# Optimization experiments

Measured on AMD Instinct MI355X. Metric: run time of the kernel, lower is better.

## Reference

```python
import jax, jax.numpy as jnp
import numpy as np
from math import exp, log

# Instant-NGP style multi-hash-grid constants (match init_kwargs)
BASE_RES = 16
MAX_RES = 2048
N_GRIDS = 16
LOG2_T = 19
TABLE_SIZE = 1 << LOG2_T  # power of two -> mod == low-bit mask
FEAT = 2
N_POINTS = 1_000_000

_pls = exp((log(MAX_RES) - log(BASE_RES)) / (N_GRIDS - 1))
RESOLUTIONS = np.floor(np.array([BASE_RES * _pls ** i for i in range(N_GRIDS)])).astype(np.float32)
# 8 voxel corner offsets, i-major (i*4 + j*2 + k) like the torch VOXEL_VTX_OFFSET
OFFSETS = np.array([[i, j, k] for i in (0, 1) for j in (0, 1) for k in (0, 1)], dtype=np.int32)
PRIMES = np.array([1, 2654435761, 805459861], dtype=np.uint32)


def setup_inputs() -> dict:
    key = jax.random.key(0)
    k1, k2 = jax.random.split(key)
    x = jax.random.normal(k1, (N_POINTS, 3), dtype=jnp.float32)
    # nn.init.uniform_(weight, a=-1e-4, b=1e-4)
    tables = jax.random.uniform(k2, (N_GRIDS, TABLE_SIZE, FEAT),
                                minval=-1e-4, maxval=1e-4, dtype=jnp.float32)
    return {"x": x, "tables": tables}


def _forward(x, tables):
    inbox = jnp.all((x >= -1.0) & (x <= 1.0), axis=-1)  # [B]
    offs = jnp.asarray(OFFSETS)                          # [8,3]
    primes = jnp.asarray(PRIMES)                         # [3] uint32
    res = jnp.asarray(RESOLUTIONS)                       # [G]
    # torch computes x_normed / interp weights under no_grad -> no grad to x
    xs = jax.lax.stop_gradient(x)

    def level(table, r):
        # (x - bbox_min) / (bbox_max - bbox_min) * resolution, bbox = [-1,1]^3
        xn = (xs + 1.0) * 0.5 * r                        # [B,3]
        v0 = jnp.floor(xn).astype(jnp.int32)             # [B,3]
        w = xn - v0.astype(jnp.float32)                  # [B,3] trilerp weights
        vidx = (v0[:, None, :] + offs[None]).astype(jnp.uint32)  # [B,8,3]
        # prime-XOR spatial hash; uint32 wraparound matches torch int64 math
        # modulo the power-of-two table size (low bits identical)
        h = (vidx[..., 0] * primes[0]) ^ (vidx[..., 1] * primes[1]) ^ (vidx[..., 2] * primes[2])
        h = (h & jnp.uint32(TABLE_SIZE - 1)).astype(jnp.int32)   # [B,8]
        feats = table[h]                                  # [B,8,F] gather
        # corner (i,j,k) weight = prod over dims of (w if bit else 1-w)
        wgt = jnp.prod(jnp.where(offs[None] == 1, w[:, None, :], 1.0 - w[:, None, :]), axis=-1)  # [B,8]
        c = jnp.einsum('bc,bcf->bf', wgt, feats)          # [B,F]
        return jnp.where(inbox[:, None], c, 0.0)          # out-of-bbox -> zeros

    per_level = jax.vmap(level)(tables, res)              # [G,B,F]
    B = x.shape[0]
    return jnp.transpose(per_level, (1, 0, 2)).reshape(B, N_GRIDS * FEAT)


def reference(x, tables):
    return _forward(x, tables)
```

## Files before the change

kernel.cpp:

```cpp
#include <hip/hip_runtime.h>
#include <hip/hip_bf16.h>
#include <math.h>

#define N_POINTS 1000000
#define N_GRIDS  16
#define LOG2_T   19
#define TABLE_MASK ((1u << LOG2_T) - 1u)
#define NBLOCKS  ((N_POINTS + 255) / 256)
#define CONV_BLOCKS 4096
#define FUSED_BLOCKS 2048
#define TAILB_BLOCKS 4096
#define N_ENTRIES (N_GRIDS << LOG2_T)
#define NCELL_AX 32
#define N_CELLS  (NCELL_AX * NCELL_AX * NCELL_AX)

struct ResArr { float r[N_GRIDS]; };

__device__ __forceinline__ unsigned pack_bf16x2(float a, float b)
{
    __hip_bfloat16 ha = __float2bfloat16(a);
    __hip_bfloat16 hb = __float2bfloat16(b);
    unsigned short ua = *(unsigned short*)&ha;
    unsigned short ub = *(unsigned short*)&hb;
    return (unsigned)ua | ((unsigned)ub << 16);
}

__device__ __forceinline__ float2 unpack_bf16x2(unsigned v)
{
    unsigned lo = (v & 0xffffu) << 16;
    unsigned hi = v & 0xffff0000u;
    return make_float2(__uint_as_float(lo), __uint_as_float(hi));
}

__device__ __forceinline__ unsigned expand_bits(unsigned v)
{
    v &= 0x3ffu;
    v = (v | (v << 16)) & 0x30000FFu;
    v = (v | (v << 8))  & 0x300F00Fu;
    v = (v | (v << 4))  & 0x30C30C3u;
    v = (v | (v << 2))  & 0x9249249u;
    return v;
}

__device__ __forceinline__ int morton_cell(float x0, float x1, float x2)
{
    int cx = (int)floorf((x0 + 1.f) * 16.f);
    int cy = (int)floorf((x1 + 1.f) * 16.f);
    int cz = (int)floorf((x2 + 1.f) * 16.f);
    cx = min(NCELL_AX - 1, max(0, cx));
    cy = min(NCELL_AX - 1, max(0, cy));
    cz = min(NCELL_AX - 1, max(0, cz));
    return (int)((expand_bits((unsigned)cx) << 2) |
                 (expand_bits((unsigned)cy) << 1) |
                  expand_bits((unsigned)cz));
}

__device__ __forceinline__ unsigned sel4(uint4 P, unsigned idx)
{
    const unsigned lo = (idx & 1u) ? P.y : P.x;
    const unsigned hi = (idx & 1u) ? P.w : P.z;
    return (idx & 2u) ? hi : lo;
}

__device__ __forceinline__ void gather_level_bf16(
    float x0, float x1, float x2, float r,
    const unsigned* __restrict__ tbl, float& c0, float& c1)
{
    const float xn0 = (x0 + 1.0f) * 0.5f * r;
    const float xn1 = (x1 + 1.0f) * 0.5f * r;
    const float xn2 = (x2 + 1.0f) * 0.5f * r;
    const float f0 = floorf(xn0), f1 = floorf(xn1), f2 = floorf(xn2);
    const unsigned v0 = (unsigned)(int)f0;
    const unsigned v1 = (unsigned)(int)f1;
    const unsigned v2 = (unsigned)(int)f2;
    const float w0 = xn0 - f0, w1 = xn1 - f1, w2 = xn2 - f2;
    const unsigned d = v0 ^ (v0 + 1u);

    unsigned sa4[4];
    uint4    pa[4];
    #pragma unroll
    for (int yz = 0; yz < 4; ++yz) {
        const unsigned vy = v1 + ((yz >> 1) & 1);
        const unsigned vz = v2 + (yz & 1);
        const unsigned m  = (vy * 2654435761u) ^ (vz * 805459861u);
        const unsigned sa = (v0 ^ m) & TABLE_MASK;
        sa4[yz] = sa;
        pa[yz]  = ((const uint4*)tbl)[sa >> 2];
    }
    const bool far = (d > 3u);
    unsigned ub[4];
    #pragma unroll
    for (int yz = 0; yz < 4; ++yz) {
        unsigned u = 0;
        if (far) u = tbl[(sa4[yz] ^ d) & TABLE_MASK];
        ub[yz] = u;
    }

    unsigned fv[8];
    #pragma unroll
    for (int yz = 0; yz < 4; ++yz) {
        const unsigned ia = sa4[yz] & 3u;
        const unsigned ib = (sa4[yz] ^ d) & 3u;
        const unsigned uA = sel4(pa[yz], ia);
        const unsigned uB = far ? ub[yz] : sel4(pa[yz], ib);
        fv[yz]     = uA;
        fv[4 + yz] = uB;
    }

    c0 = 0.f; c1 = 0.f;
    #pragma unroll
    for (int k = 0; k < 8; ++k) {
        const float wgt = ((k & 4) ? w0 : 1.0f - w0) *
                          ((k & 2) ? w1 : 1.0f - w1) *
                          ((k & 1) ? w2 : 1.0f - w2);
        const float2 f = unpack_bf16x2(fv[k]);
        c0 += wgt * f.x;
        c1 += wgt * f.y;
    }
}

__global__ __launch_bounds__(256)
void hist_kernel(const float* __restrict__ x, int* __restrict__ rank,
                 unsigned* __restrict__ hist, float* __restrict__ out)
{
    const int p = blockIdx.x * 256 + threadIdx.x;
    if (p >= N_POINTS) return;
    const float x0 = x[3 * p], x1 = x[3 * p + 1], x2 = x[3 * p + 2];
    const bool inbox = (x0 >= -1.f) & (x0 <= 1.f) &
                       (x1 >= -1.f) & (x1 <= 1.f) &
                       (x2 >= -1.f) & (x2 <= 1.f);
    if (inbox) {
        const int cell = morton_cell(x0, x1, x2);
        atomicAdd(&hist[cell], 1u);
        rank[p] = cell;
    } else {
        rank[p] = -1;
        float4* __restrict__ row = (float4*)out + (size_t)p * 8;
        const float4 z = make_float4(0.f, 0.f, 0.f, 0.f);
        #pragma unroll
        for (int i = 0; i < 8; ++i) row[i] = z;
    }
}

__global__ __launch_bounds__(1024)
void scan_kernel(unsigned* __restrict__ hist, unsigned* __restrict__ counter)
{
    __shared__ unsigned partial[1024];
    const int tid = threadIdx.x;
    uint4* __restrict__ hp = (uint4*)hist + tid * 8;
    uint4 vv[8];
    unsigned s = 0;
    #pragma unroll
    for (int i = 0; i < 8; ++i) {
        vv[i] = hp[i];
        s += vv[i].x + vv[i].y + vv[i].z + vv[i].w;
    }
    partial[tid] = s;
    __syncthreads();
    for (int off = 1; off < 1024; off <<= 1) {
        unsigned t = (tid >= off) ? partial[tid - off] : 0u;
        __syncthreads();
        partial[tid] += t;
        __syncthreads();
    }
    if (tid == 1023) counter[0] = partial[1023];
    unsigned run = partial[tid] - s;
    #pragma unroll
    for (int i = 0; i < 8; ++i) {
        uint4 o;
        o.x = run; run += vv[i].x;
        o.y = run; run += vv[i].y;
        o.z = run; run += vv[i].z;
        o.w = run; run += vv[i].w;
        hp[i] = o;
    }
}

__global__ __launch_bounds__(256)
void scatter_conv_kernel(const float* __restrict__ tables,
                         unsigned* __restrict__ tb,
                         const float* __restrict__ x,
                         const int* __restrict__ rank,
                         float4* __restrict__ xw, unsigned* __restrict__ hist)
{
    if (blockIdx.x < CONV_BLOCKS) {
        const unsigned nthr = CONV_BLOCKS * 256;
        for (unsigned e4 = blockIdx.x * 256 + threadIdx.x; e4 < (N_ENTRIES / 4);
             e4 += nthr) {
            const float4 a = ((const float4*)tables)[2 * e4];
            const float4 b = ((const float4*)tables)[2 * e4 + 1];
            uint4 o;
            o.x = pack_bf16x2(a.x, a.y);
            o.y = pack_bf16x2(a.z, a.w);
            o.z = pack_bf16x2(b.x, b.y);
            o.w = pack_bf16x2(b.z, b.w);
            ((uint4*)tb)[e4] = o;
        }
    } else {
        const int p = (blockIdx.x - CONV_BLOCKS) * 256 + threadIdx.x;
        if (p >= N_POINTS) return;
        const int cell = rank[p];
        if (cell < 0) return;
        const unsigned rk = atomicAdd(&hist[cell], 1u);
        xw[rk] = make_float4(x[3 * p], x[3 * p + 1], x[3 * p + 2],
                             __int_as_float(p));
    }
}

__global__ __launch_bounds__(256)
void fused_levels_kernel(const float4* __restrict__ xw,
                         const unsigned* __restrict__ counter,
                         const unsigned* __restrict__ tb,
                         unsigned* __restrict__ ws2, ResArr res)
{
    const unsigned k    = blockIdx.x & 7;
    const unsigned bix  = blockIdx.x >> 3;
    const unsigned nbx  = gridDim.x >> 3;
    const unsigned cnt  = *counter;
    const unsigned per  = (cnt + nbx - 1) / nbx;
    const unsigned lo   = bix * per;
    const unsigned hi   = min(cnt, lo + per);

    #pragma unroll 1
    for (int t = 0; t < 2; ++t) {
        const int g = t ? (15 - (int)k) : (int)k;
        const float r = res.r[g];
        const unsigned* __restrict__ tbl = tb + ((size_t)g << LOG2_T);
        unsigned* __restrict__ wrow = ws2 + (size_t)g * N_POINTS;
        for (unsigned i = lo + threadIdx.x; i < hi; i += 256) {
            const float4 v = xw[i];
            float c0, c1;
            gather_level_bf16(v.x, v.y, v.z, r, tbl, c0, c1);
            wrow[i] = pack_bf16x2(c0, c1);
        }
    }
}

__global__ __launch_bounds__(256)
void tail_kernel(const float4* __restrict__ xw,
                 const unsigned* __restrict__ counter,
                 const unsigned* __restrict__ ws2, float* __restrict__ out)
{
    const int t = threadIdx.x;
    const unsigned cnt = *counter;
    const unsigned tot = cnt * 8u;
    for (unsigned tg = blockIdx.x * 256 + t; tg < tot;
         tg += TAILB_BLOCKS * 256) {
        const unsigned i = tg >> 3, q = tg & 7;
        const unsigned a = ws2[(size_t)(2 * q) * N_POINTS + i];
        const unsigned b = ws2[(size_t)(2 * q + 1) * N_POINTS + i];
        const int p = __float_as_int(xw[i].w);
        const float2 fa = unpack_bf16x2(a);
        const float2 fb = unpack_bf16x2(b);
        ((float4*)out)[(size_t)p * 8 + q] =
            make_float4(fa.x, fa.y, fb.x, fb.y);
    }
}

__device__ __forceinline__ void gather_level_f32(
    float x0, float x1, float x2, float r,
    const float2* __restrict__ tbl, float& c0, float& c1)
{
    const float xn0 = (x0 + 1.0f) * 0.5f * r;
    const float xn1 = (x1 + 1.0f) * 0.5f * r;
    const float xn2 = (x2 + 1.0f) * 0.5f * r;
    const float f0 = floorf(xn0), f1 = floorf(xn1), f2 = floorf(xn2);
    const unsigned v0 = (unsigned)(int)f0;
    const unsigned v1 = (unsigned)(int)f1;
    const unsigned v2 = (unsigned)(int)f2;
    const float w0 = xn0 - f0, w1 = xn1 - f1, w2 = xn2 - f2;
    c0 = 0.f; c1 = 0.f;
    #pragma unroll
    for (int k = 0; k < 8; ++k) {
        const unsigned vx = v0 + ((k >> 2) & 1);
        const unsigned vy = v1 + ((k >> 1) & 1);
        const unsigned vz = v2 + (k & 1);
        unsigned h = (vx * 1u) ^ (vy * 2654435761u) ^ (vz * 805459861u);
        h &= TABLE_MASK;
        const float wgt = ((k & 4) ? w0 : 1.0f - w0) *
                          ((k & 2) ? w1 : 1.0f - w1) *
                          ((k & 1) ? w2 : 1.0f - w2);
        const float2 f = tbl[h];
        c0 += wgt * f.x;
        c1 += wgt * f.y;
    }
}

__global__ __launch_bounds__(256)
void mono_kernel(const float* __restrict__ x, const float* __restrict__ tables,
                 float* __restrict__ out, ResArr res)
{
    int idx = blockIdx.x * blockDim.x + threadIdx.x;
    if (idx >= N_POINTS * N_GRIDS) return;
    int b = idx >> 4, g = idx & 15;
    float x0 = x[b * 3], x1 = x[b * 3 + 1], x2 = x[b * 3 + 2];
    bool inbox = (x0 >= -1.f) & (x0 <= 1.f) & (x1 >= -1.f) & (x1 <= 1.f) &
                 (x2 >= -1.f) & (x2 <= 1.f);
    float c0 = 0.f, c1 = 0.f;
    if (inbox) {
        const float2* tbl = (const float2*)tables + ((size_t)g << LOG2_T);
        gather_level_f32(x0, x1, x2, res.r[g], tbl, c0, c1);
    }
    ((float2*)out)[(size_t)b * N_GRIDS + g] = make_float2(c0, c1);
}

extern "C" void kernel_launch(void* const* d_in, const int* in_sizes, int n_in,
                              void* d_out, int out_size, void* d_ws, size_t ws_size,
                              hipStream_t stream)
{
    const float* x      = (const float*)d_in[0];
    const float* tables = (const float*)d_in[1];
    float* out          = (float*)d_out;

    ResArr res;
    double pls = exp((log(2048.0) - log(16.0)) / 15.0);
    for (int i = 0; i < N_GRIDS; ++i)
        res.r[i] = (float)floor(16.0 * pow(pls, (double)i));

    const size_t off_hist = 256;
    const size_t off_rank = off_hist + (size_t)N_CELLS * 4;
    const size_t off_xw   = off_rank + (size_t)N_POINTS * 4;
    const size_t off_ws2  = off_xw + (size_t)N_POINTS * 16;
    const size_t off_tb   = off_ws2 + (size_t)N_GRIDS * N_POINTS * 4;
    const size_t ws_needed = off_tb + (size_t)N_ENTRIES * 4;

    if (ws_size < ws_needed) {
        int total = N_POINTS * N_GRIDS;
        mono_kernel<<<(total + 255) / 256, 256, 0, stream>>>(x, tables, out, res);
        return;
    }

    char* w = (char*)d_ws;
    unsigned* counter = (unsigned*)w;
    unsigned* hist    = (unsigned*)(w + off_hist);
    int*      rank    = (int*)(w + off_rank);
    float4*   xw      = (float4*)(w + off_xw);
    unsigned* ws2     = (unsigned*)(w + off_ws2);
    unsigned* tb      = (unsigned*)(w + off_tb);

    (void)hipMemsetAsync(w, 0, off_rank, stream);
    hist_kernel<<<NBLOCKS, 256, 0, stream>>>(x, rank, hist, out);
    scan_kernel<<<1, 1024, 0, stream>>>(hist, counter);
    scatter_conv_kernel<<<CONV_BLOCKS + NBLOCKS, 256, 0, stream>>>(
        tables, tb, x, rank, xw, hist);
    fused_levels_kernel<<<FUSED_BLOCKS, 256, 0, stream>>>(xw, counter, tb,
                                                          ws2, res);
    tail_kernel<<<TAILB_BLOCKS, 256, 0, stream>>>(xw, counter, ws2, out);
}
```

Before: 172.2 us.

## Move table conversion into histogram pass and zero out-of-box rows in level kernel

New measurement: 180.9 us. 1.05x slower.

```diff
diff --git a/kernel.cpp b/kernel.cpp
--- a/kernel.cpp
+++ b/kernel.cpp
@@ -120,68 +120,9 @@
 }
 
 __global__ __launch_bounds__(256)
-void hist_kernel(const float* __restrict__ x, int* __restrict__ rank,
-                 unsigned* __restrict__ hist, float* __restrict__ out)
-{
-    const int p = blockIdx.x * 256 + threadIdx.x;
-    if (p >= N_POINTS) return;
-    const float x0 = x[3 * p], x1 = x[3 * p + 1], x2 = x[3 * p + 2];
-    const bool inbox = (x0 >= -1.f) & (x0 <= 1.f) &
-                       (x1 >= -1.f) & (x1 <= 1.f) &
-                       (x2 >= -1.f) & (x2 <= 1.f);
-    if (inbox) {
-        const int cell = morton_cell(x0, x1, x2);
-        atomicAdd(&hist[cell], 1u);
-        rank[p] = cell;
-    } else {
-        rank[p] = -1;
-        float4* __restrict__ row = (float4*)out + (size_t)p * 8;
-        const float4 z = make_float4(0.f, 0.f, 0.f, 0.f);
-        #pragma unroll
-        for (int i = 0; i < 8; ++i) row[i] = z;
-    }
-}
-
-__global__ __launch_bounds__(1024)
-void scan_kernel(unsigned* __restrict__ hist, unsigned* __restrict__ counter)
-{
-    __shared__ unsigned partial[1024];
-    const int tid = threadIdx.x;
-    uint4* __restrict__ hp = (uint4*)hist + tid * 8;
-    uint4 vv[8];
-    unsigned s = 0;
-    #pragma unroll
-    for (int i = 0; i < 8; ++i) {
-        vv[i] = hp[i];
-        s += vv[i].x + vv[i].y + vv[i].z + vv[i].w;
-    }
-    partial[tid] = s;
-    __syncthreads();
-    for (int off = 1; off < 1024; off <<= 1) {
-        unsigned t = (tid >= off) ? partial[tid - off] : 0u;
-        __syncthreads();
-        partial[tid] += t;
-        __syncthreads();
-    }
-    if (tid == 1023) counter[0] = partial[1023];
-    unsigned run = partial[tid] - s;
-    #pragma unroll
-    for (int i = 0; i < 8; ++i) {
-        uint4 o;
-        o.x = run; run += vv[i].x;
-        o.y = run; run += vv[i].y;
-        o.z = run; run += vv[i].z;
-        o.w = run; run += vv[i].w;
-        hp[i] = o;
-    }
-}
-
-__global__ __launch_bounds__(256)
-void scatter_conv_kernel(const float* __restrict__ tables,
-                         unsigned* __restrict__ tb,
-                         const float* __restrict__ x,
-                         const int* __restrict__ rank,
-                         float4* __restrict__ xw, unsigned* __restrict__ hist)
+void prep_kernel(const float* __restrict__ tables, unsigned* __restrict__ tb,
+                 const float* __restrict__ x, int* __restrict__ rank,
+                 unsigned* __restrict__ hist)
 {
     if (blockIdx.x < CONV_BLOCKS) {
         const unsigned nthr = CONV_BLOCKS * 256;
@@ -199,19 +140,74 @@
     } else {
         const int p = (blockIdx.x - CONV_BLOCKS) * 256 + threadIdx.x;
         if (p >= N_POINTS) return;
-        const int cell = rank[p];
-        if (cell < 0) return;
-        const unsigned rk = atomicAdd(&hist[cell], 1u);
-        xw[rk] = make_float4(x[3 * p], x[3 * p + 1], x[3 * p + 2],
-                             __int_as_float(p));
-    }
+        const float x0 = x[3 * p], x1 = x[3 * p + 1], x2 = x[3 * p + 2];
+        const bool inbox = (x0 >= -1.f) & (x0 <= 1.f) &
+                           (x1 >= -1.f) & (x1 <= 1.f) &
+                           (x2 >= -1.f) & (x2 <= 1.f);
+        if (inbox) {
+            const int cell = morton_cell(x0, x1, x2);
+            atomicAdd(&hist[cell], 1u);
+            rank[p] = cell;
+        } else {
+            rank[p] = -1;
+        }
+    }
+}
+
+__global__ __launch_bounds__(1024)
+void scan_kernel(unsigned* __restrict__ hist, unsigned* __restrict__ counter)
+{
+    __shared__ unsigned partial[1024];
+    const int tid = threadIdx.x;
+    uint4* __restrict__ hp = (uint4*)hist + tid * 8;
+    uint4 vv[8];
+    unsigned s = 0;
+    #pragma unroll
+    for (int i = 0; i < 8; ++i) {
+        vv[i] = hp[i];
+        s += vv[i].x + vv[i].y + vv[i].z + vv[i].w;
+    }
+    partial[tid] = s;
+    __syncthreads();
+    for (int off = 1; off < 1024; off <<= 1) {
+        unsigned t = (tid >= off) ? partial[tid - off] : 0u;
+        __syncthreads();
+        partial[tid] += t;
+        __syncthreads();
+    }
+    if (tid == 1023) counter[0] = partial[1023];
+    unsigned run = partial[tid] - s;
+    #pragma unroll
+    for (int i = 0; i < 8; ++i) {
+        uint4 o;
+        o.x = run; run += vv[i].x;
+        o.y = run; run += vv[i].y;
+        o.z = run; run += vv[i].z;
+        o.w = run; run += vv[i].w;
+        hp[i] = o;
+    }
+}
+
+__global__ __launch_bounds__(256)
+void scatter_kernel(const float* __restrict__ x, const int* __restrict__ rank,
+                    float4* __restrict__ xw, unsigned* __restrict__ hist)
+{
+    const int p = blockIdx.x * 256 + threadIdx.x;
+    if (p >= N_POINTS) return;
+    const int cell = rank[p];
+    if (cell < 0) return;
+    const unsigned rk = atomicAdd(&hist[cell], 1u);
+    xw[rk] = make_float4(x[3 * p], x[3 * p + 1], x[3 * p + 2],
+                         __int_as_float(p));
 }
 
 __global__ __launch_bounds__(256)
 void fused_levels_kernel(const float4* __restrict__ xw,
                          const unsigned* __restrict__ counter,
                          const unsigned* __restrict__ tb,
-                         unsigned* __restrict__ ws2, ResArr res)
+                         unsigned* __restrict__ ws2, ResArr res,
+                         const int* __restrict__ rank,
+                         float* __restrict__ out)
 {
     const unsigned k    = blockIdx.x & 7;
     const unsigned bix  = blockIdx.x >> 3;
@@ -232,6 +228,22 @@
             float c0, c1;
             gather_level_bf16(v.x, v.y, v.z, r, tbl, c0, c1);
             wrow[i] = pack_bf16x2(c0, c1);
+        }
+    }
+
+    if (k < 5) {
+        const unsigned li   = k * nbx + bix;
+        const unsigned nli  = 5 * nbx;
+        const unsigned zper = (N_POINTS + nli - 1) / nli;
+        const unsigned p0   = li * zper;
+        const unsigned p1   = min((unsigned)N_POINTS, p0 + zper);
+        const float4 z = make_float4(0.f, 0.f, 0.f, 0.f);
+        for (unsigned p = p0 + threadIdx.x; p < p1; p += 256) {
+            if (rank[p] < 0) {
+                float4* __restrict__ row = (float4*)out + (size_t)p * 8;
+                #pragma unroll
+                for (int i = 0; i < 8; ++i) row[i] = z;
+            }
         }
     }
 }
@@ -339,11 +351,11 @@
     unsigned* tb      = (unsigned*)(w + off_tb);
 
     (void)hipMemsetAsync(w, 0, off_rank, stream);
-    hist_kernel<<<NBLOCKS, 256, 0, stream>>>(x, rank, hist, out);
+    prep_kernel<<<CONV_BLOCKS + NBLOCKS, 256, 0, stream>>>(
+        tables, tb, x, rank, hist);
     scan_kernel<<<1, 1024, 0, stream>>>(hist, counter);
-    scatter_conv_kernel<<<CONV_BLOCKS + NBLOCKS, 256, 0, stream>>>(
-        tables, tb, x, rank, xw, hist);
-    fused_levels_kernel<<<FUSED_BLOCKS, 256, 0, stream>>>(xw, counter, tb,
-                                                          ws2, res);
+    scatter_kernel<<<NBLOCKS, 256, 0, stream>>>(x, rank, xw, hist);
+    fused_levels_kernel<<<FUSED_BLOCKS, 256, 0, stream>>>(
+        xw, counter, tb, ws2, res, rank, out);
     tail_kernel<<<TAILB_BLOCKS, 256, 0, stream>>>(xw, counter, ws2, out);
 }
```
